# Kernel optimization log

Hardware: AMD Instinct MI355X
Metric: run time of the kernel (lower is better)

Reference implementation:

```python
import jax, jax.numpy as jnp
import numpy as np
import math

EMBED_DIM = 1024
NHEAD = 16
HD = EMBED_DIM // NHEAD      # 64
HHD = HD // 2                # 32
LAMBDA_INIT = 0.8
LN_EPS = 1e-5
B, T = 2, 2048


def setup_inputs() -> dict:
    key = jax.random.key(0)
    ks = jax.random.split(key, 12)
    d = EMBED_DIM
    inp = {
        "x": jax.random.normal(ks[0], (B, T, d), dtype=jnp.float32),
        "key_padding_mask": jnp.zeros((B, T), dtype=bool),
        "Wq": jax.random.normal(ks[1], (d, d), dtype=jnp.float32) / math.sqrt(d),
        "Wk": jax.random.normal(ks[2], (d, d), dtype=jnp.float32) / math.sqrt(d),
        "Wv": jax.random.normal(ks[3], (d, d), dtype=jnp.float32) / math.sqrt(d),
        "Wo": jax.random.normal(ks[4], (d, d), dtype=jnp.float32) / math.sqrt(d),
        "gamma": jnp.ones((d,), dtype=jnp.float32),
        "beta": jnp.zeros((d,), dtype=jnp.float32),
        "lq1": jax.random.normal(ks[5], (NHEAD, HHD), dtype=jnp.float32) * 0.1,
        "lk1": jax.random.normal(ks[6], (NHEAD, HHD), dtype=jnp.float32) * 0.1,
        "lq2": jax.random.normal(ks[7], (NHEAD, HHD), dtype=jnp.float32) * 0.1,
        "lk2": jax.random.normal(ks[8], (NHEAD, HHD), dtype=jnp.float32) * 0.1,
    }
    return inp


def _diff_attn(x, key_padding_mask, Wq, Wk, Wv, Wo, gamma, beta, lq1, lk1, lq2, lk2):
    b, t, d = x.shape
    scale = math.sqrt(HHD)

    def split(w):  # [B,T,D] -> [B,H,T,hd]
        return w.reshape(b, t, NHEAD, HD).transpose(0, 2, 1, 3)

    Q = split(x @ Wq.T)
    K = split(x @ Wk.T)
    V = split(x @ Wv.T)
    Q1, Q2 = Q[..., :HHD], Q[..., HHD:]
    K1, K2 = K[..., :HHD], K[..., HHD:]

    def attn(q, k):  # [B,H,T,hhd] x [B,H,T,hhd] -> softmax scores [B,H,T,T]
        scores = jnp.einsum('bhqe,bhke->bhqk', q, k) / scale
        scores = jnp.where(key_padding_mask[:, None, None, :], -jnp.inf, scores)
        return jax.nn.softmax(scores, axis=-1)

    lam = (jnp.exp(jnp.sum(lq1 * lk1, axis=-1))
           - jnp.exp(jnp.sum(lq2 * lk2, axis=-1))
           + LAMBDA_INIT)  # [H]
    A = attn(Q1, K1) - lam[None, :, None, None] * attn(Q2, K2)
    out = jnp.einsum('bhqk,bhkd->bhqd', A, V).transpose(0, 2, 1, 3).reshape(b, t, d)
    y = out @ Wo.T + x
    mu = jnp.mean(y, axis=-1, keepdims=True)
    var = jnp.mean((y - mu) ** 2, axis=-1, keepdims=True)
    return (y - mu) / jnp.sqrt(var + LN_EPS) * gamma + beta


def reference(x, key_padding_mask, Wq, Wk, Wv, Wo, gamma, beta, lq1, lk1, lq2, lk2):
    return _diff_attn(x, key_padding_mask, Wq, Wk, Wv, Wo, gamma, beta, lq1, lk1, lq2, lk2)
```

## Files before the change

kernel.cpp:

```cpp
#include <hip/hip_runtime.h>
#include <stdint.h>

#define DEVI __device__ __forceinline__

typedef __bf16 bf16x8 __attribute__((ext_vector_type(8)));
typedef float f32x4 __attribute__((ext_vector_type(4)));
typedef unsigned short u16x8 __attribute__((ext_vector_type(8)));
typedef unsigned u32x2 __attribute__((ext_vector_type(2)));
typedef unsigned u32x4 __attribute__((ext_vector_type(4)));

#define MFMA16(a, b, c) __builtin_amdgcn_mfma_f32_16x16x32_bf16((a), (b), (c), 0, 0, 0)

constexpr int EMBED = 1024;
constexpr int NHEADC = 16;
constexpr int BB = 2;
constexpr int TT = 2048;
constexpr int MROWS = BB * TT;
constexpr int QKSTR = 2048;
constexpr float QSCALE = 0.17677669529663687f * 1.4426950408889634f;

DEVI unsigned short f2bf(float f) {
  unsigned u = __float_as_uint(f);
  u += 0x7fffu + ((u >> 16) & 1u);
  return (unsigned short)(u >> 16);
}
DEVI unsigned cvtpk(float lo, float hi) {
  unsigned pk;
  asm("v_cvt_pk_bf16_f32 %0, %1, %2" : "=v"(pk) : "v"(lo), "v"(hi));
  return pk;
}

DEVI void gl2lds16(const void* g, void* l) {
  __builtin_amdgcn_global_load_lds(
      (const __attribute__((address_space(1))) void*)(uintptr_t)g,
      (__attribute__((address_space(3))) void*)(unsigned)(uintptr_t)l,
      16, 0, 0);
}

DEVI void split_body(const float* in, unsigned short* hi, int n4, int start, int stride) {
  for (int i = start; i < n4; i += stride) {
    float4 v = reinterpret_cast<const float4*>(in)[i];
    ushort4 h;
    h.x = f2bf(v.x); h.y = f2bf(v.y); h.z = f2bf(v.z); h.w = f2bf(v.w);
    reinterpret_cast<ushort4*>(hi)[i] = h;
  }
}

__global__ __launch_bounds__(256) void k_splitall(
    const float* __restrict__ x, const float* __restrict__ Wq,
    const float* __restrict__ Wk, const float* __restrict__ Wv,
    const float* __restrict__ Wo, unsigned short* __restrict__ xhi,
    unsigned short* __restrict__ wqkv, unsigned short* __restrict__ woh) {
  const int bid = blockIdx.x;
  if (bid < 1024) {
    split_body(x, xhi, MROWS * EMBED / 4, bid * 256 + threadIdx.x, 1024 * 256);
  } else {
    const int y = (bid - 1024) >> 7;
    const int lb = (bid - 1024) & 127;
    const float* in = (y == 0) ? Wq : (y == 1) ? Wk : (y == 2) ? Wv : Wo;
    unsigned short* hi = (y == 3) ? woh : wqkv + (size_t)y * EMBED * EMBED;
    split_body(in, hi, EMBED * EMBED / 4, lb * 256 + threadIdx.x, 128 * 256);
  }
}

template <int EPI>
__global__ __launch_bounds__(256) void k_gemm(
    const unsigned short* __restrict__ Ahi, const unsigned short* __restrict__ Bhi,
    unsigned short* __restrict__ O1, unsigned short* __restrict__ O2,
    float* __restrict__ Of32, const float* __restrict__ resid,
    int M, int N, int K, int ldo, float oscale) {
  __shared__ __align__(16) unsigned short sAh[128 * 64];
  __shared__ __align__(16) unsigned short sBh[128 * 64];

  const int tid = threadIdx.x;
  const int lane = tid & 63;
  const int w = tid >> 6;
  const int arow = lane & 15;
  const int g = lane >> 4;

  int bm, bn;
  {
    const int q = blockIdx.x & 7;
    const int idx = blockIdx.x >> 3;
    if constexpr (EPI == 4) {
      bm = ((q >> 1) * 8 + idx / 12) * 128;
      bn = ((q & 1) * 12 + idx % 12) * 128;
    } else {
      bm = (q * 4 + idx / 8) * 128;
      bn = (idx % 8) * 128;
    }
  }
  const int wr = (w >> 1) * 64;
  const int wc = (w & 1) * 64;

  const f32x4 z4 = {0.f, 0.f, 0.f, 0.f};
  f32x4 acc[4][4];
#pragma unroll
  for (int i = 0; i < 4; ++i)
#pragma unroll
    for (int j = 0; j < 4; ++j) acc[i][j] = z4;

  for (int k0 = 0; k0 < K; k0 += 64) {
    __syncthreads();
#pragma unroll
    for (int i = 0; i < 4; ++i) {
      const int cid = (i * 4 + w) * 64 + lane;
      const int r = cid >> 3;
      const int c = cid & 7;
      const int sc = (c ^ (r & 7)) * 8;
      const int ldso = (i * 4 + w) * 512;
      gl2lds16(Ahi + (size_t)(bm + r) * K + k0 + sc, &sAh[ldso]);
      gl2lds16(Bhi + (size_t)(bn + r) * K + k0 + sc, &sBh[ldso]);
    }
    __syncthreads();
#pragma unroll
    for (int kk = 0; kk < 2; ++kk) {
      bf16x8 ah[4], bh[4];
#pragma unroll
      for (int mi = 0; mi < 4; ++mi) {
        const int row = wr + mi * 16 + arow;
        const int ch = ((kk * 4 + g) ^ (row & 7)) * 8;
        ah[mi] = *reinterpret_cast<const bf16x8*>(&sAh[row * 64 + ch]);
      }
#pragma unroll
      for (int ni = 0; ni < 4; ++ni) {
        const int row = wc + ni * 16 + arow;
        const int ch = ((kk * 4 + g) ^ (row & 7)) * 8;
        bh[ni] = *reinterpret_cast<const bf16x8*>(&sBh[row * 64 + ch]);
      }
#pragma unroll
      for (int mi = 0; mi < 4; ++mi)
#pragma unroll
        for (int ni = 0; ni < 4; ++ni)
          acc[mi][ni] = MFMA16(ah[mi], bh[ni], acc[mi][ni]);
    }
  }

#pragma unroll
  for (int mi = 0; mi < 4; ++mi)
#pragma unroll
    for (int ni = 0; ni < 4; ++ni)
#pragma unroll
      for (int r = 0; r < 4; ++r) {
        const int row = bm + wr + mi * 16 + g * 4 + r;
        const int col = bn + wc + ni * 16 + arow;
        float f = acc[mi][ni][r];
        if constexpr (EPI == 2) {
          const size_t idx = (size_t)row * ldo + col;
          Of32[idx] = f + resid[idx];
        } else {
          if (col < 2048) {
            O1[(size_t)row * 2048 + col] = f2bf(col < 1024 ? f * oscale : f);
          } else {
            O2[(size_t)row * 1024 + (col - 2048)] = f2bf(f);
          }
        }
      }
}

__global__ __launch_bounds__(256, 4) void k_attn(
    const unsigned short* __restrict__ QKhi, const unsigned short* __restrict__ Vb,
    unsigned short* __restrict__ Out,
    const float* __restrict__ lq1, const float* __restrict__ lk1,
    const float* __restrict__ lq2, const float* __restrict__ lk2) {
  __shared__ __align__(16) unsigned short sK[2][64 * 64];
  __shared__ __align__(16) unsigned short sVt[64 * 64];

  const int tid = threadIdx.x;
  const int lane = tid & 63;
  const int w = tid >> 6;
  const int ten = w >> 1;
  const int qc = w & 1;
  const int arow = lane & 15;
  const int g = lane >> 4;

  const int lin = blockIdx.x;
  const int m_ = lin >> 3;
  const int bh = ((m_ >> 6) << 3) | (lin & 7);
  const int qx = m_ & 63;
  const int q0 = qx * 32;
  const int b = bh >> 4;
  const int h = bh & 15;

  const int r0 = tid >> 3;
  const int c0 = tid & 7;
  const unsigned short* kg =
      QKhi + (size_t)(b * TT + r0) * QKSTR + 1024 + h * 64 + ((c0 ^ (r0 & 7)) * 8);
  const size_t kgj = (size_t)32 * QKSTR;
  unsigned short* const kda = &sK[0][w * 512];
  unsigned short* const kdb = &sK[0][2048 + w * 512];
  unsigned short* const kda1 = &sK[1][w * 512];
  unsigned short* const kdb1 = &sK[1][2048 + w * 512];

  const int tp = tid >> 3;
  const int vc = tid & 7;
  const unsigned short* vg = Vb + (size_t)(b * TT + 2 * tp) * EMBED + h * 64 + vc * 8;
  unsigned vwoff[8];
#pragma unroll
  for (int i = 0; i < 8; ++i) {
    const int d = vc * 8 + i;
    const int fd = (i ^ vc) & 7;
    vwoff[i] = d * 128 + ((tp ^ (fd << 2)) << 2);
  }
  unsigned koff[4];
#pragma unroll
  for (int n = 0; n < 4; ++n) {
    const int krow = n * 16 + arow;
    koff[n] = (krow * 64 + ((g + 4 * ten) ^ (krow & 7)) * 8) * 2;
  }
  unsigned vfoff[8];
#pragma unroll
  for (int kk = 0; kk < 2; ++kk)
#pragma unroll
    for (int n = 0; n < 4; ++n) {
      const int vr = n * 16 + arow;
      const int fd = (vr ^ (vr >> 3)) & 7;
      vfoff[kk * 4 + n] = vr * 128 + ((kk * 4 + g) ^ fd) * 16;
    }

  u16x8 va0, va1, na0, na1;
  gl2lds16(kg, kda);
  gl2lds16(kg + kgj, kdb);
  va0 = *reinterpret_cast<const u16x8*>(vg);
  va1 = *reinterpret_cast<const u16x8*>(vg + EMBED);
  kg += (size_t)64 * QKSTR;
  vg += (size_t)64 * EMBED;

  const int qrow = q0 + qc * 16 + arow;
  const bf16x8 qh = *reinterpret_cast<const bf16x8*>(
      &QKhi[(size_t)(b * TT + qrow) * QKSTR + h * 64 + ten * 32 + g * 8]);

  float d1 = 0.f, d2 = 0.f;
#pragma unroll
  for (int i = 0; i < 32; ++i) {
    d1 += lq1[h * 32 + i] * lk1[h * 32 + i];
    d2 += lq2[h * 32 + i] * lk2[h * 32 + i];
  }
  const float lam = __expf(d1) - __expf(d2) + 0.8f;

  const f32x4 z4 = {0.f, 0.f, 0.f, 0.f};
  const u32x4 ones4 = {0x3F803F80u, 0x3F803F80u, 0x3F803F80u, 0x3F803F80u};
  const bf16x8 onev = __builtin_bit_cast(bf16x8, ones4);
  f32x4 o[4], ol;
#pragma unroll
  for (int n = 0; n < 4; ++n) o[n] = z4;
  ol = z4;

  const char* const svt = reinterpret_cast<const char*>(sVt);

#define ATTN_TILE(T, KOFF, KDa, KDb)                                                 \
  do {                                                                               \
    __syncthreads();                  \
    if ((T) + 1 < TT / 64) {                                                         \
      gl2lds16(kg, (KDa));                                                           \
      gl2lds16(kg + kgj, (KDb));                                                     \
      na0 = *reinterpret_cast<const u16x8*>(vg);                                     \
      na1 = *reinterpret_cast<const u16x8*>(vg + EMBED);                             \
      kg += (size_t)64 * QKSTR;                                                      \
      vg += (size_t)64 * EMBED;                                                      \
      asm volatile("s_waitcnt vmcnt(4)" ::: "memory");                               \
    } else {                                                                         \
      asm volatile("s_waitcnt vmcnt(0)" ::: "memory");                               \
    }                                                                                \
    {                   \
      char* vb8 = reinterpret_cast<char*>(sVt);                                      \
      const u32x4 pd0 = __builtin_bit_cast(u32x4, va0);                              \
      const u32x4 pd1 = __builtin_bit_cast(u32x4, va1);                              \
      _Pragma("unroll") for (int dw = 0; dw < 4; ++dw) {                             \
        const unsigned pe = __builtin_amdgcn_perm(pd1[dw], pd0[dw], 0x05040100);     \
        const unsigned po = __builtin_amdgcn_perm(pd1[dw], pd0[dw], 0x07060302);     \
        *reinterpret_cast<unsigned*>(vb8 + vwoff[2 * dw]) = pe;                      \
        *reinterpret_cast<unsigned*>(vb8 + vwoff[2 * dw + 1]) = po;                  \
      }                                                                              \
    }                                                                                \
    __syncthreads();                                                \
    f32x4 s[4];                                                                      \
    __builtin_amdgcn_s_setprio(1);                                                   \
    _Pragma("unroll") for (int n = 0; n < 4; ++n) {                                  \
      const bf16x8 kh = *reinterpret_cast<const bf16x8*>(                            \
          reinterpret_cast<const char*>(&sK[0][0]) + (KOFF) + koff[n]);              \
      s[n] = MFMA16(kh, qh, z4);                                                     \
    }                                                                                \
    __builtin_amdgcn_s_setprio(0);                                                   \
    unsigned pk[4][2];                                                               \
    _Pragma("unroll") for (int n = 0; n < 4; ++n) {                                  \
      const float p0 = __builtin_amdgcn_exp2f(s[n][0]);                              \
      const float p1 = __builtin_amdgcn_exp2f(s[n][1]);                              \
      const float p2 = __builtin_amdgcn_exp2f(s[n][2]);                              \
      const float p3 = __builtin_amdgcn_exp2f(s[n][3]);                              \
      pk[n][0] = cvtpk(p0, p1);                                                      \
      pk[n][1] = cvtpk(p2, p3);                                                      \
    }                                                                                \
    bf16x8 pf[2];                                                                    \
    _Pragma("unroll") for (int kk = 0; kk < 2; ++kk) {                               \
      unsigned u0 = pk[2 * kk][0], w0 = pk[2 * kk + 1][0];                           \
      asm("v_permlane32_swap_b32 %0, %1" : "+v"(u0), "+v"(w0));                      \
      asm("v_permlane16_swap_b32 %0, %1" : "+v"(u0), "+v"(w0));                      \
      unsigned u1 = pk[2 * kk][1], w1 = pk[2 * kk + 1][1];                           \
      asm("v_permlane32_swap_b32 %0, %1" : "+v"(u1), "+v"(w1));                      \
      asm("v_permlane16_swap_b32 %0, %1" : "+v"(u1), "+v"(w1));                      \
      const u32x4 q4 = {u0, u1, w0, w1};                                             \
      pf[kk] = __builtin_bit_cast(bf16x8, q4);                                       \
    }                                                                                \
    __builtin_amdgcn_s_setprio(1);                                                   \
    _Pragma("unroll") for (int kk = 0; kk < 2; ++kk) {                               \
      ol = MFMA16(onev, pf[kk], ol);                \
      _Pragma("unroll") for (int n = 0; n < 4; ++n) {                                \
        const bf16x8 vf =                                                            \
            *reinterpret_cast<const bf16x8*>(svt + vfoff[kk * 4 + n]);               \
        o[n] = MFMA16(vf, pf[kk], o[n]);                                             \
      }                                                                              \
    }                                                                                \
    __builtin_amdgcn_s_setprio(0);                                                   \
    va0 = na0;                                                                       \
    va1 = na1;                                                                       \
  } while (0)

  for (int tt = 0; tt < TT / 128; ++tt) {
    ATTN_TILE(2 * tt, 0, kda1, kdb1);
    ATTN_TILE(2 * tt + 1, 8192, kda, kdb);
  }
#undef ATTN_TILE

  const float lsum = ol[0];

  float* sComb = reinterpret_cast<float*>(&sK[0][0]);
  __syncthreads();
  if (ten == 1) {
    const float rl2 = lam / lsum;
#pragma unroll
    for (int n = 0; n < 4; ++n)
#pragma unroll
      for (int r = 0; r < 4; ++r)
        sComb[(qc * 16 + arow) * 72 + n * 16 + g * 4 + r] = o[n][r] * rl2;
  }
  __syncthreads();
  if (ten == 0) {
    const float rl1 = 1.f / lsum;
    const size_t orow = (size_t)(b * TT + q0 + qc * 16 + arow) * EMBED + h * 64;
    const float* cb = &sComb[(qc * 16 + arow) * 72];
#pragma unroll
    for (int n = 0; n < 4; ++n) {
      const float v0 = o[n][0] * rl1 - cb[n * 16 + g * 4 + 0];
      const float v1 = o[n][1] * rl1 - cb[n * 16 + g * 4 + 1];
      const float v2 = o[n][2] * rl1 - cb[n * 16 + g * 4 + 2];
      const float v3 = o[n][3] * rl1 - cb[n * 16 + g * 4 + 3];
      u32x2 pk2;
      pk2[0] = cvtpk(v0, v1);
      pk2[1] = cvtpk(v2, v3);
      *reinterpret_cast<u32x2*>(&Out[orow + n * 16 + g * 4]) = pk2;
    }
  }
}

__global__ __launch_bounds__(256) void k_ln(const float* __restrict__ y,
                                            const float* __restrict__ gamma,
                                            const float* __restrict__ beta,
                                            float* __restrict__ out) {
  __shared__ float red[2][4];
  const int row = blockIdx.x;
  const int tid = threadIdx.x;
  const int lane = tid & 63;
  const int w = tid >> 6;
  float4 v = reinterpret_cast<const float4*>(y + (size_t)row * 1024)[tid];
  float s = v.x + v.y + v.z + v.w;
  float q = v.x * v.x + v.y * v.y + v.z * v.z + v.w * v.w;
#pragma unroll
  for (int mask = 32; mask >= 1; mask >>= 1) {
    s += __shfl_xor(s, mask, 64);
    q += __shfl_xor(q, mask, 64);
  }
  if (lane == 0) { red[0][w] = s; red[1][w] = q; }
  __syncthreads();
  s = red[0][0] + red[0][1] + red[0][2] + red[0][3];
  q = red[1][0] + red[1][1] + red[1][2] + red[1][3];
  const float mu = s * (1.f / 1024.f);
  const float var = q * (1.f / 1024.f) - mu * mu;
  const float rstd = rsqrtf(var + 1e-5f);
  const float4 gm = reinterpret_cast<const float4*>(gamma)[tid];
  const float4 bt = reinterpret_cast<const float4*>(beta)[tid];
  float4 o;
  o.x = (v.x - mu) * rstd * gm.x + bt.x;
  o.y = (v.y - mu) * rstd * gm.y + bt.y;
  o.z = (v.z - mu) * rstd * gm.z + bt.z;
  o.w = (v.w - mu) * rstd * gm.w + bt.w;
  reinterpret_cast<float4*>(out + (size_t)row * 1024)[tid] = o;
}

extern "C" void kernel_launch(void* const* d_in, const int* in_sizes, int n_in,
                              void* d_out, int out_size, void* d_ws, size_t ws_size,
                              hipStream_t stream) {
  const float* x = (const float*)d_in[0];
  const float* Wq = (const float*)d_in[2];
  const float* Wk = (const float*)d_in[3];
  const float* Wv = (const float*)d_in[4];
  const float* Wo = (const float*)d_in[5];
  const float* gamma = (const float*)d_in[6];
  const float* beta = (const float*)d_in[7];
  const float* lq1 = (const float*)d_in[8];
  const float* lk1 = (const float*)d_in[9];
  const float* lq2 = (const float*)d_in[10];
  const float* lk2 = (const float*)d_in[11];

  size_t off = 0;
  auto wsalloc = [&](size_t bytes) -> void* {
    void* p = (char*)d_ws + off;
    off += (bytes + 255) & ~(size_t)255;
    return p;
  };
  const size_t actb = (size_t)MROWS * EMBED * 2;
  const size_t wtb = (size_t)EMBED * EMBED * 2;
  const size_t qkb = (size_t)MROWS * QKSTR * 2;
  unsigned short* xhi = (unsigned short*)wsalloc(actb);
  unsigned short* wqkv = (unsigned short*)wsalloc(3 * wtb);
  unsigned short* woh = (unsigned short*)wsalloc(wtb);
  unsigned short* qkh = (unsigned short*)wsalloc(qkb);
  unsigned short* vb = (unsigned short*)wsalloc(actb);
  unsigned short* ao = (unsigned short*)wsalloc(actb);
  float* yf = (float*)wsalloc((size_t)MROWS * EMBED * 4);

  k_splitall<<<1536, 256, 0, stream>>>(x, Wq, Wk, Wv, Wo, xhi, wqkv, woh);

  k_gemm<4><<<768, 256, 0, stream>>>(
      xhi, wqkv, qkh, vb, nullptr, nullptr, MROWS, 3072, EMBED, 0, QSCALE);

  k_attn<<<2048, 256, 0, stream>>>(qkh, vb, ao, lq1, lk1, lq2, lk2);

  k_gemm<2><<<256, 256, 0, stream>>>(
      ao, woh, nullptr, nullptr, yf, x, MROWS, 1024, EMBED, 1024, 1.f);

  k_ln<<<MROWS, 256, 0, stream>>>(yf, gamma, beta, (float*)d_out);
}
```

Baseline: 160.0 us.

## Deepen attention K/V pipeline to four K buffers and two V buffers, one barrier per tile

Replaces the double-buffered K tile and single V-transpose buffer with a 48KB LDS pool holding four K stages and two V-transposed buffers. Prefetch is issued two tiles ahead, after the barrier, which removes the second __syncthreads per tile. The cost is more LDS per block (48KB vs 24KB), which may lower occupancy below the 4 blocks per CU requested in launch bounds. It also keeps more registers live for the two in-flight V fragments.

```diff
diff --git a/kernel.cpp b/kernel.cpp
--- a/kernel.cpp
+++ b/kernel.cpp
@@ -163,8 +163,7 @@
     unsigned short* __restrict__ Out,
     const float* __restrict__ lq1, const float* __restrict__ lk1,
     const float* __restrict__ lq2, const float* __restrict__ lk2) {
-  __shared__ __align__(16) unsigned short sK[2][64 * 64];
-  __shared__ __align__(16) unsigned short sVt[64 * 64];
+  __shared__ __align__(16) char sPool[49152];
 
   const int tid = threadIdx.x;
   const int lane = tid & 63;
@@ -187,10 +186,7 @@
   const unsigned short* kg =
       QKhi + (size_t)(b * TT + r0) * QKSTR + 1024 + h * 64 + ((c0 ^ (r0 & 7)) * 8);
   const size_t kgj = (size_t)32 * QKSTR;
-  unsigned short* const kda = &sK[0][w * 512];
-  unsigned short* const kdb = &sK[0][2048 + w * 512];
-  unsigned short* const kda1 = &sK[1][w * 512];
-  unsigned short* const kdb1 = &sK[1][2048 + w * 512];
+  char* const kdw = sPool + w * 1024;
 
   const int tp = tid >> 3;
   const int vc = tid & 7;
@@ -218,11 +214,17 @@
       vfoff[kk * 4 + n] = vr * 128 + ((kk * 4 + g) ^ fd) * 16;
     }
 
-  u16x8 va0, va1, na0, na1;
-  gl2lds16(kg, kda);
-  gl2lds16(kg + kgj, kdb);
-  va0 = *reinterpret_cast<const u16x8*>(vg);
-  va1 = *reinterpret_cast<const u16x8*>(vg + EMBED);
+  u16x8 vaA0, vaA1, vaB0, vaB1;
+  gl2lds16(kg, kdw);
+  gl2lds16(kg + kgj, kdw + 4096);
+  vaA0 = *reinterpret_cast<const u16x8*>(vg);
+  vaA1 = *reinterpret_cast<const u16x8*>(vg + EMBED);
+  kg += (size_t)64 * QKSTR;
+  vg += (size_t)64 * EMBED;
+  gl2lds16(kg, kdw + 8192);
+  gl2lds16(kg + kgj, kdw + 8192 + 4096);
+  vaB0 = *reinterpret_cast<const u16x8*>(vg);
+  vaB1 = *reinterpret_cast<const u16x8*>(vg + EMBED);
   kg += (size_t)64 * QKSTR;
   vg += (size_t)64 * EMBED;
 
@@ -246,39 +248,33 @@
   for (int n = 0; n < 4; ++n) o[n] = z4;
   ol = z4;
 
-  const char* const svt = reinterpret_cast<const char*>(sVt);
-
-#define ATTN_TILE(T, KOFF, KDa, KDb)                                                 \
+#define ATTN_TILE(VM, DOSTAGE, KOFF, NXTOFF, VOFF, VA0, VA1)                         \
   do {                                                                               \
-    __syncthreads();                  \
-    if ((T) + 1 < TT / 64) {                                                         \
-      gl2lds16(kg, (KDa));                                                           \
-      gl2lds16(kg + kgj, (KDb));                                                     \
-      na0 = *reinterpret_cast<const u16x8*>(vg);                                     \
-      na1 = *reinterpret_cast<const u16x8*>(vg + EMBED);                             \
-      kg += (size_t)64 * QKSTR;                                                      \
-      vg += (size_t)64 * EMBED;                                                      \
-      asm volatile("s_waitcnt vmcnt(4)" ::: "memory");                               \
-    } else {                                                                         \
-      asm volatile("s_waitcnt vmcnt(0)" ::: "memory");                               \
-    }                                                                                \
-    {                   \
-      char* vb8 = reinterpret_cast<char*>(sVt);                                      \
-      const u32x4 pd0 = __builtin_bit_cast(u32x4, va0);                              \
-      const u32x4 pd1 = __builtin_bit_cast(u32x4, va1);                              \
+    asm volatile("s_waitcnt vmcnt(" VM ")" ::: "memory");                            \
+    {                                       \
+      const u32x4 pd0 = __builtin_bit_cast(u32x4, VA0);                              \
+      const u32x4 pd1 = __builtin_bit_cast(u32x4, VA1);                              \
       _Pragma("unroll") for (int dw = 0; dw < 4; ++dw) {                             \
         const unsigned pe = __builtin_amdgcn_perm(pd1[dw], pd0[dw], 0x05040100);     \
         const unsigned po = __builtin_amdgcn_perm(pd1[dw], pd0[dw], 0x07060302);     \
-        *reinterpret_cast<unsigned*>(vb8 + vwoff[2 * dw]) = pe;                      \
-        *reinterpret_cast<unsigned*>(vb8 + vwoff[2 * dw + 1]) = po;                  \
+        *reinterpret_cast<unsigned*>(sPool + (VOFF) + vwoff[2 * dw]) = pe;           \
+        *reinterpret_cast<unsigned*>(sPool + (VOFF) + vwoff[2 * dw + 1]) = po;       \
       }                                                                              \
     }                                                                                \
-    __syncthreads();                                                \
+    __syncthreads();         \
+    if (DOSTAGE) {              \
+      gl2lds16(kg, kdw + (NXTOFF));                                                  \
+      gl2lds16(kg + kgj, kdw + (NXTOFF) + 4096);                                     \
+      VA0 = *reinterpret_cast<const u16x8*>(vg);                                     \
+      VA1 = *reinterpret_cast<const u16x8*>(vg + EMBED);                             \
+      kg += (size_t)64 * QKSTR;                                                      \
+      vg += (size_t)64 * EMBED;                                                      \
+    }                                                                                \
     f32x4 s[4];                                                                      \
     __builtin_amdgcn_s_setprio(1);                                                   \
     _Pragma("unroll") for (int n = 0; n < 4; ++n) {                                  \
-      const bf16x8 kh = *reinterpret_cast<const bf16x8*>(                            \
-          reinterpret_cast<const char*>(&sK[0][0]) + (KOFF) + koff[n]);              \
+      const bf16x8 kh =                                                              \
+          *reinterpret_cast<const bf16x8*>(sPool + (KOFF) + koff[n]);                \
       s[n] = MFMA16(kh, qh, z4);                                                     \
     }                                                                                \
     __builtin_amdgcn_s_setprio(0);                                                   \
@@ -306,25 +302,29 @@
     _Pragma("unroll") for (int kk = 0; kk < 2; ++kk) {                               \
       ol = MFMA16(onev, pf[kk], ol);                \
       _Pragma("unroll") for (int n = 0; n < 4; ++n) {                                \
-        const bf16x8 vf =                                                            \
-            *reinterpret_cast<const bf16x8*>(svt + vfoff[kk * 4 + n]);               \
+        const bf16x8 vf = *reinterpret_cast<const bf16x8*>(                          \
+            sPool + (VOFF) + vfoff[kk * 4 + n]);                                     \
         o[n] = MFMA16(vf, pf[kk], o[n]);                                             \
       }                                                                              \
     }                                                                                \
     __builtin_amdgcn_s_setprio(0);                                                   \
-    va0 = na0;                                                                       \
-    va1 = na1;                                                                       \
   } while (0)
 
-  for (int tt = 0; tt < TT / 128; ++tt) {
-    ATTN_TILE(2 * tt, 0, kda1, kdb1);
-    ATTN_TILE(2 * tt + 1, 8192, kda, kdb);
-  }
+  for (int tt = 0; tt < 7; ++tt) {
+    ATTN_TILE("4", 1, 0, 16384, 32768, vaA0, vaA1);
+    ATTN_TILE("4", 1, 8192, 24576, 40960, vaB0, vaB1);
+    ATTN_TILE("4", 1, 16384, 0, 32768, vaA0, vaA1);
+    ATTN_TILE("4", 1, 24576, 8192, 40960, vaB0, vaB1);
+  }
+  ATTN_TILE("4", 1, 0, 16384, 32768, vaA0, vaA1);
+  ATTN_TILE("4", 1, 8192, 24576, 40960, vaB0, vaB1);
+  ATTN_TILE("4", 0, 16384, 0, 32768, vaA0, vaA1);
+  ATTN_TILE("0", 0, 24576, 0, 40960, vaB0, vaB1);
 #undef ATTN_TILE
 
   const float lsum = ol[0];
 
-  float* sComb = reinterpret_cast<float*>(&sK[0][0]);
+  float* sComb = reinterpret_cast<float*>(sPool);
   __syncthreads();
   if (ten == 1) {
     const float rl2 = lam / lsum;
```

Result: slower. 169.5 us (+6.0%).
